# Optimization experiments

Measured on AMD Instinct MI355X. Metric: run time of the kernel, lower is better.

Reference implementation:

```python
import jax, jax.numpy as jnp
import numpy as np

B0, K, H, W = 8, 1, 512, 512
S, CS, NMS, M = 25, 51, 5, 2048
REG_W, COV_POW = 1.0, 0.5

def _gauss_kernel(n):
    x = jnp.linspace(-1.0, 1.0, n)
    g = jnp.exp(-x * x / 0.5)
    return g / g.sum()

def _conv1d2d(x, k1d, horizontal, pad_h, pad_w):
    # x: [B,1,H,W]; replicates torch F.conv2d with the given (possibly asymmetric) padding
    kern = k1d.reshape(1, 1, 1, -1) if horizontal else k1d.reshape(1, 1, -1, 1)
    return jax.lax.conv_general_dilated(x, kern, (1, 1), [(pad_h, pad_h), (pad_w, pad_w)],
                                        dimension_numbers=("NCHW", "OIHW", "NCHW"))

def bilinear_sample(img, pts):
    # img [B,C,H,W], pts [B,N,2] (x,y in [-1,1]); grid_sample bilinear, align_corners=False, zero padding
    Bb, C, Hh, Ww = img.shape
    x = (pts[..., 0] + 1.0) * 0.5 * Ww - 0.5
    y = (pts[..., 1] + 1.0) * 0.5 * Hh - 0.5
    x0 = jnp.floor(x); y0 = jnp.floor(y)
    wx = x - x0; wy = y - y0
    x0i = x0.astype(jnp.int32); y0i = y0.astype(jnp.int32)
    flat = img.reshape(Bb, C, Hh * Ww)
    def tap(yi, xi, w):
        ok = ((yi >= 0) & (yi < Hh) & (xi >= 0) & (xi < Ww)).astype(img.dtype)
        idx = jnp.clip(yi, 0, Hh - 1) * Ww + jnp.clip(xi, 0, Ww - 1)  # [B,N]
        v = jnp.take_along_axis(flat, idx[:, None, :], axis=2)        # [B,C,N]
        return v * (w * ok)[:, None, :]
    return (tap(y0i, x0i, (1 - wy) * (1 - wx)) + tap(y0i, x0i + 1, (1 - wy) * wx)
            + tap(y0i + 1, x0i, wy * (1 - wx)) + tap(y0i + 1, x0i + 1, wy * wx))

def compute_matchability(keypoint_p, has_depth, Bt):
    G = _gauss_kernel(S)
    # NOTE: faithful to original asymmetric padding bug: pad H while convolving along W, then pad W while convolving along H
    s = _conv1d2d(keypoint_p.reshape(Bt, 1, H, W), G, True, S // 2, 0)
    s = _conv1d2d(s, G, False, 0, S // 2)
    log_p_hat = jax.nn.log_softmax(jnp.log(s.reshape(Bt, H * W) + 1e-8), axis=-1)
    sd = _conv1d2d(has_depth.reshape(Bt, 1, H, W), G, True, 0, S // 2)
    sd = _conv1d2d(sd, G, False, S // 2, 0).reshape(Bt, H * W)
    p = sd / sd.sum(-1, keepdims=True)
    return jnp.sum(jnp.where(p > 0, p * (jnp.log(jnp.maximum(p, 1e-30)) - log_p_hat), 0.0), axis=-1)

def sample_keypoints(sm):
    # sm [B,H,W]; coverage-reweighted NMS + top-k (topk=True, subpixel=False)
    wcov = jnp.exp(-jnp.square(jnp.linspace(-2.0, 2.0, CS)))
    ld = _conv1d2d(((sm + 1e-6) * 1e4)[:, None], wcov, True, 0, CS // 2)
    ld = _conv1d2d(ld, wcov, False, CS // 2, 0)[:, 0]
    sm = sm * (ld + 1e-8) ** (-COV_POW)
    p = NMS // 2
    mx = jax.lax.reduce_window(sm, -jnp.inf, jax.lax.max, (1, NMS, NMS), (1, 1, 1),
                               [(0, 0), (p, p), (p, p)])
    sm = sm * (sm == mx)
    _, inds = jax.lax.top_k(sm.reshape(-1, H * W), M)
    xs = (jnp.arange(W) + 0.5) * 2.0 / W - 1.0
    ys = (jnp.arange(H) + 0.5) * 2.0 / H - 1.0
    grid = jnp.stack(jnp.meshgrid(xs, ys, indexing="xy"), axis=-1).reshape(H * W, 2)
    return jnp.take(grid, inds, axis=0)  # [B,M,2] normalized (x,y)

def masked_log_softmax(logits, mask):
    return jax.nn.log_softmax(jnp.where(mask, logits, -1e9), axis=-1)

def _reward(d):
    return jnp.exp(-100.0 * d)

def _forward(scoremap, gt_warp_A2B, gt_warp_B2A, valid_A2B, valid_B2A, has_depth):
    sg = jax.lax.stop_gradient
    lA = scoremap[:B0].reshape(B0, K, H * W)
    lB = scoremap[B0:].reshape(B0, K, H * W)
    logits = jnp.concatenate([lA, lB], 0)                                   # [2B,K,HW]
    kp_p = jax.nn.softmax(logits.reshape(2 * B0, K * H * W), -1).reshape(2 * B0, K, H * W).sum(1)
    match_loss = compute_matchability(kp_p, sg(has_depth), 2 * B0).mean()
    # sparse branch is under torch.set_grad_enabled(False)
    kpts_A = sample_keypoints(sg(kp_p[:B0]).reshape(B0, H, W))
    kpts_B = sample_keypoints(sg(kp_p[B0:]).reshape(B0, H, W))
    kpts_A2B = bilinear_sample(sg(gt_warp_A2B[..., 2:]).transpose(0, 3, 1, 2), kpts_A).transpose(0, 2, 1)
    kpts_B2A = bilinear_sample(sg(gt_warp_B2A[..., 2:]).transpose(0, 3, 1, 2), kpts_B).transpose(0, 2, 1)
    legit_A2B = bilinear_sample(sg(valid_A2B)[:, None], kpts_A)[:, 0] > 0   # [B,M]
    legit_B2A = bilinear_sample(sg(valid_B2A)[:, None], kpts_B)[:, 0] > 0
    dA = jnp.sqrt(jnp.sum(jnp.square(kpts_A2B[:, :, None] - kpts_B[:, None]), -1) + 1e-12).min(-1)
    dB = jnp.sqrt(jnp.sum(jnp.square(kpts_B2A[:, :, None] - kpts_A[:, None]), -1) + 1e-12).min(-1)
    rA = _reward(dA); rB = _reward(dB)
    slA = bilinear_sample(lA.reshape(B0, 1, H, W), kpts_A)[:, 0]            # [B,M]
    slB = bilinear_sample(lB.reshape(B0, 1, H, W), kpts_B)[:, 0]
    lpA = masked_log_softmax(slA, legit_A2B)
    lpB = masked_log_softmax(slB, legit_B2A)
    sparse = -jnp.sum(jnp.where(legit_A2B, rA * lpA, 0.0)) - jnp.sum(jnp.where(legit_B2A, rB * lpB, 0.0))
    return sparse + REG_W * match_loss

def setup_inputs() -> dict:
    key = jax.random.key(0)
    ks = jax.random.split(key, 6)
    scoremap = jax.random.normal(ks[0], (2 * B0, K, H, W), jnp.float32)
    gt_warp_A2B = jax.random.uniform(ks[1], (B0, H, W, 4), jnp.float32, -1.0, 1.0)
    gt_warp_B2A = jax.random.uniform(ks[2], (B0, H, W, 4), jnp.float32, -1.0, 1.0)
    valid_A2B = (jax.random.uniform(ks[3], (B0, H, W)) > 0.3).astype(jnp.float32)
    valid_B2A = (jax.random.uniform(ks[4], (B0, H, W)) > 0.3).astype(jnp.float32)
    has_depth = (jax.random.uniform(ks[5], (2 * B0, H, W)) > 0.3).astype(jnp.float32)
    return dict(scoremap=scoremap, gt_warp_A2B=gt_warp_A2B, gt_warp_B2A=gt_warp_B2A,
                valid_A2B=valid_A2B, valid_B2A=valid_B2A, has_depth=has_depth)

def reference(scoremap, gt_warp_A2B, gt_warp_B2A, valid_A2B, valid_B2A, has_depth):
    return _forward(scoremap, gt_warp_A2B, gt_warp_B2A, valid_A2B, valid_B2A, has_depth)
```

## Files before the change

kernel.cpp:

```cpp
#include <hip/hip_runtime.h>

#define HH 512
#define WW 512
#define HW_ 262144
#define NIMG 16
#define MK 2048
#define CAPB 4096
#define SCAP 32768
#define SBUFN 768

static constexpr size_t OFF_B1    = 16777216;
static constexpr size_t OFF_B2    = 33554432;
static constexpr size_t OFF_SMALL = 50331648;
static constexpr size_t OFF_SEL  = 4194304;
static constexpr size_t OFF_BND  = 4325376;
static constexpr size_t OFF_PP   = 4849664;
static constexpr size_t OFF_WXp  = 5111808;
static constexpr size_t OFF_WYp  = 5242880;
static constexpr size_t OFF_LG   = 5373952;
static constexpr size_t OFF_SL   = 5505024;
static constexpr size_t OFF_PMIN = 5636096;
static constexpr size_t OFF_HIST = 33554432;
static constexpr size_t OFF_SURV = 33554432 + 4194304;

#define CSTRIDE 32

__device__ __forceinline__ float wred64(float v) {
  for (int m = 1; m < 64; m <<= 1) v += __shfl_xor(v, m);
  return v;
}

__device__ __forceinline__ void g25_wave0(float* g) {
  int t = threadIdx.x;
  if (t < 64) {
    float raw = 0.0f;
    if (t < 25) {
      float x = -1.0f + (float)t * (2.0f / 24.0f);
      raw = expf(-(x * x) / 0.5f);
    }
    float s = raw;
    for (int m = 1; m < 64; m <<= 1) s += __shfl_xor(s, m);
    if (t < 25) g[t] = raw / s;
  }
}
__device__ __forceinline__ void w51_wave0(float* wc) {
  int t = threadIdx.x;
  if (t < 51) {
    float x = -2.0f + (float)t * (4.0f / 50.0f);
    wc[t] = expf(-x * x);
  }
}

template<int B>
__device__ __forceinline__ float brsum(float v, float* red) {
  int t = threadIdx.x;
  red[t] = v; __syncthreads();
  for (int s = B >> 1; s > 0; s >>= 1) {
    if (t < s) red[t] += red[t + s];
    __syncthreads();
  }
  float r = red[0]; __syncthreads();
  return r;
}
template<int B>
__device__ __forceinline__ float brmax(float v, float* red) {
  int t = threadIdx.x;
  red[t] = v; __syncthreads();
  for (int s = B >> 1; s > 0; s >>= 1) {
    if (t < s) red[t] = fmaxf(red[t], red[t + s]);
    __syncthreads();
  }
  float r = red[0]; __syncthreads();
  return r;
}

__global__ void __launch_bounds__(256)
k_pre(const float* __restrict__ x, const float* __restrict__ hd, float* A,
      float* sume, float* sumS, float* Zb) {
  __shared__ float g[25];
  __shared__ float red[12];
  int tid = threadIdx.x;
  g25_wave0(g);
  size_t base = (size_t)blockIdx.x * 1024;
  size_t e = base + tid * 4;
  float4 xs = *(const float4*)(x + e);
  float4 hs = *(const float4*)(hd + e);
  __syncthreads();
  int rem = (int)(e & (HW_ - 1));
  int y = rem >> 9, x0 = rem & 511;
  float wv = 0.0f;
  {
    int k0 = y - 499; if (k0 < 0) k0 = 0;
    int k1 = y + 12;  if (k1 > 24) k1 = 24;
    for (int k = k0; k <= k1; k++) wv += g[k];
  }
  float cwv[4], cpv[4];
  {
    int lo = x0 - 487; if (lo < 0) lo = 0;
    int hi = x0;       if (hi > 24) hi = 24;
    float c = 0.0f;
    for (int d = lo; d <= hi; d++) c += g[d];
    cwv[0] = c;
    for (int q = 1; q < 4; q++) {
      int i = x0 + q;
      if (i <= 24) c += g[i];
      if (i >= 488) c -= g[i - 488];
      cwv[q] = c;
    }
  }
  {
    int lo = x0 - 499; if (lo < 0) lo = 0;
    int hi = x0 + 12;  if (hi > 24) hi = 24;
    float c = 0.0f;
    for (int d = lo; d <= hi; d++) c += g[d];
    cpv[0] = c;
    for (int q = 1; q < 4; q++) {
      int i = x0 + q;
      if (i + 12 <= 24) c += g[i + 12];
      if (i >= 500) c -= g[i - 500];
      cpv[q] = c;
    }
  }
  float e0 = expf(xs.x), e1 = expf(xs.y), e2 = expf(xs.z), e3 = expf(xs.w);
  *(float4*)(A + e) = make_float4(e0, e1, e2, e3);
  float r0 = (e0 + e1) + (e2 + e3);
  float r1 = (e0 * cwv[0] + e1 * cwv[1] + e2 * cwv[2] + e3 * cwv[3]) * wv;
  float r2 = (hs.x * cpv[0] + hs.y * cpv[1] + hs.z * cpv[2] + hs.w * cpv[3]) * wv;
  r0 = wred64(r0); r1 = wred64(r1); r2 = wred64(r2);
  int wid = tid >> 6;
  if ((tid & 63) == 0) { red[wid] = r0; red[4 + wid] = r1; red[8 + wid] = r2; }
  __syncthreads();
  if (tid == 0) {
    int img = (int)(base >> 18);
    atomicAdd(&sume[img * CSTRIDE], red[0] + red[1] + red[2] + red[3]);
    atomicAdd(&sumS[img * CSTRIDE], red[4] + red[5] + red[6] + red[7]);
    atomicAdd(&Zb[img * CSTRIDE], red[8] + red[9] + red[10] + red[11]);
  }
}

__global__ void __launch_bounds__(256)
k_hconv(const float* __restrict__ A, const float* __restrict__ hd,
        const float* __restrict__ sume, float* b1, float* b2) {
  __shared__ __align__(16) float ta[512];
  __shared__ __align__(16) float th[536];
  __shared__ float g[25];
  int tid = threadIdx.x;
  int blk = blockIdx.x;
  int img = blk >> 9;
  size_t rowoff = (size_t)blk * 512;
  g25_wave0(g);
  ((float2*)ta)[tid] = *(const float2*)(A + rowoff + tid * 2);
  ((float2*)(th + 12))[tid] = *(const float2*)(hd + rowoff + tid * 2);
  if (tid < 12) { th[tid] = 0.0f; th[524 + tid] = 0.0f; }
  __syncthreads();
  float inv = 1.0f / sume[img * CSTRIDE];
  int j = 2 * tid;
  float v1a = 0.0f, v1b = 0.0f;
  if (tid >= 6 && tid <= 249) {
    float w[26];
#pragma unroll
    for (int d = 0; d < 26; d++) w[d] = ta[j - 12 + d];
#pragma unroll
    for (int d = 0; d < 25; d++) {
      v1a = fmaf(g[d], w[d], v1a);
      v1b = fmaf(g[d], w[d + 1], v1b);
    }
  }
  float v2a = 0.0f, v2b = 0.0f;
  {
    float u[26];
#pragma unroll
    for (int d = 0; d < 26; d++) u[d] = th[j + d];
#pragma unroll
    for (int d = 0; d < 25; d++) {
      v2a = fmaf(g[d], u[d], v2a);
      v2b = fmaf(g[d], u[d + 1], v2b);
    }
  }
  ((float2*)b1)[blk * 256 + tid] = make_float2(v1a * inv, v1b * inv);
  ((float2*)b2)[blk * 256 + tid] = make_float2(v2a, v2b);
}

__global__ void __launch_bounds__(256)
k_match(const float* __restrict__ b1, const float* __restrict__ b2,
        const float* __restrict__ sume, const float* sumS, const float* Zb,
        float* macc) {
  __shared__ float g[25];
  __shared__ float t1[88 * 64];
  __shared__ float t2[88 * 64];
  __shared__ float red4[4];
  g25_wave0(g);
  int blk = blockIdx.x;
  int img = blk >> 6;
  int ty = (blk >> 3) & 7;
  int tx = blk & 7;
  int y0 = ty * 64, x0 = tx * 64;
  const float* base1 = b1 + (size_t)img * HW_;
  const float* base2 = b2 + (size_t)img * HW_;
  for (int i = threadIdx.x; i < 88 * 64; i += 256) {
    int r = i >> 6, c = i & 63;
    int y = y0 + r - 12;
    float v1 = 0.0f, v2 = 0.0f;
    if (y >= 0 && y < 512) {
      size_t o = (size_t)y * 512 + x0 + c;
      v1 = base1[o]; v2 = base2[o];
    }
    t1[i] = v1; t2[i] = v2;
  }
  __syncthreads();
  float Z = Zb[img * CSTRIDE];
  float inv = 1.0f / sume[img * CSTRIDE];
  float logS = logf(sumS[img * CSTRIDE] * inv + (float)HW_ * 1e-8f);
  float acc = 0.0f;
  for (int w = threadIdx.x; w < 1024; w += 256) {
    int rg = w >> 6, c = w & 63;
    int r0 = rg * 4;
    float s[4] = {0.f, 0.f, 0.f, 0.f};
    float d[4] = {0.f, 0.f, 0.f, 0.f};
#pragma unroll
    for (int i = 0; i < 28; i++) {
      float v1 = t1[(r0 + i) * 64 + c];
      float v2 = t2[(r0 + i) * 64 + c];
#pragma unroll
      for (int jj = 0; jj < 4; jj++) {
        if (i >= jj && i - jj < 25) {
          s[jj] = fmaf(g[i - jj], v1, s[jj]);
          d[jj] = fmaf(g[i - jj], v2, d[jj]);
        }
      }
    }
#pragma unroll
    for (int jj = 0; jj < 4; jj++) {
      float p = d[jj] / Z;
      if (p > 0.0f)
        acc += p * (logf(fmaxf(p, 1e-30f)) - (logf(s[jj] + 1e-8f) - logS));
    }
  }
  acc = wred64(acc);
  if ((threadIdx.x & 63) == 0) red4[threadIdx.x >> 6] = acc;
  __syncthreads();
  if (threadIdx.x == 0)
    atomicAdd(macc, red4[0] + red4[1] + red4[2] + red4[3]);
}

__global__ void __launch_bounds__(256)
k_h51(const float* __restrict__ A, const float* __restrict__ sume, float* out) {
  __shared__ float wc[51];
  __shared__ __align__(16) float ta[564];
  int tid = threadIdx.x;
  int blk = blockIdx.x;
  int img = blk >> 9;
  size_t rowoff = (size_t)blk * 512;
  w51_wave0(wc);
  float s1 = 1e4f / sume[img * CSTRIDE];
  for (int i = tid; i < 562; i += 256) {
    int j = i - 25;
    ta[i] = ((unsigned)j < 512u) ? fmaf(A[rowoff + j], s1, 1e-2f) : 0.0f;
  }
  __syncthreads();
  int j = 2 * tid;
  float w[52];
#pragma unroll
  for (int d = 0; d < 52; d++) w[d] = ta[j + d];
  float va = 0.0f, vb = 0.0f;
#pragma unroll
  for (int d = 0; d < 51; d++) {
    va = fmaf(wc[d], w[d], va);
    vb = fmaf(wc[d], w[d + 1], vb);
  }
  ((float2*)out)[blk * 256 + tid] = make_float2(va, vb);
}

__global__ void __launch_bounds__(512)
k_smwnms(const float* __restrict__ A, const float* __restrict__ sume,
         const float* __restrict__ b1,
         unsigned long long* surv, unsigned* scnt, unsigned* hist) {
  __shared__ float wc[51];
  __shared__ float tb1[118 * 68];
  __shared__ float tsm[68 * 68];
  __shared__ unsigned long long sbuf[SBUFN];
  __shared__ unsigned lcnt;
  __shared__ unsigned gbase;
  float* hm = tb1;
  int tid = threadIdx.x;
  w51_wave0(wc);
  if (tid == 0) lcnt = 0;
  int blk = blockIdx.x;
  int img = blk >> 6;
  int ty = (blk >> 3) & 7;
  int tx = blk & 7;
  int y0 = ty * 64, x0 = tx * 64;
  const float* base = b1 + (size_t)img * HW_;
  for (int i = tid; i < 118 * 68; i += 512) {
    int r = i / 68, c = i - r * 68;
    int y = y0 + r - 27, x = x0 + c - 2;
    tb1[i] = (y >= 0 && y < 512 && x >= 0 && x < 512)
                 ? base[(size_t)y * 512 + x] : 0.0f;
  }
  __syncthreads();
  float inv = 1.0f / sume[img * CSTRIDE];
  const float* abase = A + (size_t)img * HW_;
  for (int w = tid; w < 68 * 17; w += 512) {
    int rg = w / 68, c = w - rg * 68;
    int r0 = rg * 4;
    float a[4] = {0.f, 0.f, 0.f, 0.f};
#pragma unroll
    for (int i = 0; i < 54; i++) {
      float v = tb1[(r0 + i) * 68 + c];
#pragma unroll
      for (int jj = 0; jj < 4; jj++) {
        if (i >= jj && i - jj < 51) a[jj] = fmaf(wc[i - jj], v, a[jj]);
      }
    }
#pragma unroll
    for (int jj = 0; jj < 4; jj++) {
      int r = r0 + jj;
      int y = y0 + r - 2, x = x0 + c - 2;
      float res = -3.4e38f;
      if (y >= 0 && y < 512 && x >= 0 && x < 512)
        res = (abase[(size_t)y * 512 + x] * inv) / sqrtf(a[jj] + 1e-8f);
      tsm[r * 68 + c] = res;
    }
  }
  __syncthreads();
  for (int i = tid; i < 68 * 64; i += 512) {
    int r = i >> 6, c = i & 63;
    const float* row = tsm + r * 68 + c;
    float m = fmaxf(fmaxf(row[0], row[1]), fmaxf(row[2], fmaxf(row[3], row[4])));
    hm[i] = m;
  }
  __syncthreads();
  for (int k0 = 0; k0 < 8; k0++) {
    int i = tid + k0 * 512;
    int r = i >> 6, c = i & 63;
    float v = tsm[(r + 2) * 68 + (c + 2)];
    float M = hm[r * 64 + c];
    M = fmaxf(M, hm[(r + 1) * 64 + c]);
    M = fmaxf(M, hm[(r + 2) * 64 + c]);
    M = fmaxf(M, hm[(r + 3) * 64 + c]);
    M = fmaxf(M, hm[(r + 4) * 64 + c]);
    bool keep = (v == M) && (v != 0.0f);
    if (keep) {
      unsigned p = atomicAdd(&lcnt, 1u);
      unsigned bits = __float_as_uint(v);
      unsigned idx = (unsigned)((y0 + r) * 512 + x0 + c);
      if (p < SBUFN)
        sbuf[p] = ((unsigned long long)bits << 32) |
                  (unsigned long long)(idx ^ 0xFFFFFFFFu);
      atomicAdd(&hist[(size_t)img * 65536 + (bits >> 16)], 1u);
    }
  }
  __syncthreads();
  unsigned total = lcnt; if (total > SBUFN) total = SBUFN;
  if (tid == 0) gbase = atomicAdd(&scnt[img * CSTRIDE], total);
  __syncthreads();
  unsigned gb = gbase;
  for (unsigned i = tid; i < total; i += 512) {
    unsigned p = gb + i;
    if (p < SCAP) surv[(size_t)img * SCAP + p] = sbuf[i];
  }
}

__global__ void k_thresh(const unsigned* __restrict__ hist, unsigned* Tb, unsigned* needb) {
  int img = blockIdx.x;
  const unsigned* h = hist + (size_t)img * 65536;
  __shared__ unsigned part[256];
  __shared__ unsigned scan[257];
  int t = threadIdx.x;
  unsigned s = 0;
  for (int k = 0; k < 256; k++) {
    int bin = 65535 - (t * 256 + k);
    s += (bin == 0) ? 0x00100000u : h[bin];
  }
  part[t] = s; __syncthreads();
  if (t == 0) {
    unsigned c = 0;
    for (int k = 0; k < 256; k++) { scan[k] = c; c += part[k]; }
    scan[256] = c;
  }
  __syncthreads();
  unsigned pre = scan[t];
  if (pre < MK && pre + part[t] >= MK) {
    unsigned c = pre;
    for (int k = 0; k < 256; k++) {
      int bin = 65535 - (t * 256 + k);
      unsigned cnt = (bin == 0) ? 0x00100000u : h[bin];
      if (c + cnt >= MK) { Tb[img * CSTRIDE] = (unsigned)bin; needb[img * CSTRIDE] = MK - c; break; }
      c += cnt;
    }
  }
}

__global__ void k_collect(const unsigned long long* __restrict__ surv,
                          const unsigned* __restrict__ scnt,
                          const unsigned* __restrict__ Tb,
                          unsigned* selcnt, unsigned* sel,
                          unsigned* bcnt, unsigned long long* bnd) {
  int blk = blockIdx.x;
  int img = blk >> 7;
  int i = (blk & 127) * 256 + threadIdx.x;
  unsigned cnt = scnt[img * CSTRIDE]; if (cnt > SCAP) cnt = SCAP;
  unsigned long long entry = ((unsigned)i < cnt) ? surv[(size_t)img * SCAP + i] : 0ull;
  unsigned bits = (unsigned)(entry >> 32);
  unsigned bin = bits >> 16;
  unsigned T = Tb[img * CSTRIDE];
  bool ok = (unsigned)i < cnt;
  bool c1 = ok && (bin > T);
  bool c2 = ok && (bin == T);
  int lane = threadIdx.x & 63;
  unsigned long long lowmask = (1ull << lane) - 1ull;

  unsigned long long m1 = __ballot(c1);
  if (m1) {
    int leader = __ffsll(m1) - 1;
    unsigned base = 0;
    if (lane == leader) base = atomicAdd(&selcnt[img * CSTRIDE], (unsigned)__popcll(m1));
    base = __shfl(base, leader);
    if (c1) {
      unsigned p = base + (unsigned)__popcll(m1 & lowmask);
      if (p < MK) sel[img * MK + p] = (unsigned)(entry & 0xFFFFFFFFull) ^ 0xFFFFFFFFu;
    }
  }
  unsigned long long m2 = __ballot(c2);
  if (m2) {
    int leader = __ffsll(m2) - 1;
    unsigned base = 0;
    if (lane == leader) base = atomicAdd(&bcnt[img * CSTRIDE], (unsigned)__popcll(m2));
    base = __shfl(base, leader);
    if (c2) {
      unsigned p = base + (unsigned)__popcll(m2 & lowmask);
      if (p < CAPB) bnd[(size_t)img * CAPB + p] = entry;
    }
  }
}

__global__ void __launch_bounds__(1024)
k_finsel(const unsigned long long* __restrict__ bnd, const unsigned* bcnt,
         const unsigned* needb, const unsigned* selcnt, unsigned* sel) {
  int img = blockIdx.x;
  __shared__ unsigned long long key[CAPB];
  unsigned bn = bcnt[img * CSTRIDE];
  int n = (bn < CAPB) ? (int)bn : CAPB;
  int np2 = 2;
  while (np2 < n) np2 <<= 1;
  int t = threadIdx.x;
  for (int k = t; k < np2; k += 1024)
    key[k] = (k < n) ? bnd[(size_t)img * CAPB + k] : 0ull;
  __syncthreads();
  for (int sz = 2; sz <= np2; sz <<= 1) {
    for (int st = sz >> 1; st > 0; st >>= 1) {
      for (int i = t; i < np2; i += 1024) {
        int l = i ^ st;
        if (l > i) {
          unsigned long long a = key[i], b = key[l];
          bool up = ((i & sz) == 0);
          if (up ? (a < b) : (a > b)) { key[i] = b; key[l] = a; }
        }
      }
      __syncthreads();
    }
  }
  unsigned c1 = selcnt[img * CSTRIDE]; if (c1 > MK) c1 = MK;
  unsigned need = needb[img * CSTRIDE];
  unsigned kk = need; if (kk > MK - c1) kk = MK - c1;
  for (unsigned m = t; m < MK - c1; m += 1024) {
    unsigned v = 0u;
    if (m < kk && m < (unsigned)n)
      v = (unsigned)(key[m] & 0xFFFFFFFFull) ^ 0xFFFFFFFFu;
    sel[img * MK + c1 + m] = v;
  }
}

__global__ void k_prep(const unsigned* __restrict__ sel, const float* __restrict__ scoremap,
                       const float* __restrict__ gtA, const float* __restrict__ gtB,
                       const float* __restrict__ vA, const float* __restrict__ vB,
                       float2* pp, float* wx, float* wy, float* lg, float* sl) {
  int t = blockIdx.x * 256 + threadIdx.x;
  int img = t >> 11;
  unsigned idx = sel[t] & (HW_ - 1);
  int h = idx >> 9, w = idx & 511;
  pp[t] = make_float2((w + 0.5f) * (2.0f / 512.0f) - 1.0f,
                      (h + 0.5f) * (2.0f / 512.0f) - 1.0f);
  int b = (img < 8) ? img : img - 8;
  const float* gt = (img < 8) ? gtA : gtB;
  const float* vv = (img < 8) ? vA : vB;
  size_t pix = (size_t)b * HW_ + idx;
  float2 gxy = *(const float2*)(gt + pix * 4 + 2);
  wx[t] = gxy.x;
  wy[t] = gxy.y;
  lg[t] = (vv[pix] > 0.0f) ? 1.0f : 0.0f;
  sl[t] = scoremap[(size_t)img * HW_ + idx];
}

__global__ void __launch_bounds__(256)
k_mindist(const float2* __restrict__ pp,
          const float* __restrict__ wx, const float* __restrict__ wy,
          float* pmin) {
  __shared__ float2 opp[512];
  int blk = blockIdx.x;
  int img = blk >> 5;
  int qc = (blk >> 2) & 7;
  int oc = blk & 3;
  const float2* ob = pp + (size_t)(img ^ 8) * MK + oc * 512;
  for (int k = threadIdx.x; k < 512; k += 256) opp[k] = ob[k];
  __syncthreads();
  int m = img * MK + qc * 256 + threadIdx.x;
  float ax = wx[m], ay = wy[m];
  float d[8];
#pragma unroll
  for (int u = 0; u < 8; u++) d[u] = 3.4e38f;
  for (int n = 0; n < 512; n += 8) {
#pragma unroll
    for (int u = 0; u < 8; u++) {
      float2 o = opp[n + u];
      float dx = ax - o.x, dy = ay - o.y;
      d[u] = fminf(d[u], fmaf(dx, dx, dy * dy));
    }
  }
  float d2 = fminf(fminf(fminf(d[0], d[1]), fminf(d[2], d[3])),
                   fminf(fminf(d[4], d[5]), fminf(d[6], d[7])));
  pmin[oc * (NIMG * MK) + m] = d2;
}

__global__ void __launch_bounds__(1024)
k_loss(const float* __restrict__ sl, const float* __restrict__ lg,
       const float* __restrict__ pmin, float* sacc) {
  int img = blockIdx.x;
  __shared__ float red[1024];
  int t = threadIdx.x;
  int i0 = img * MK + t, i1 = i0 + 1024;
  float s0 = sl[i0], s1 = sl[i1];
  float g0 = lg[i0], g1 = lg[i1];
  float l0 = (g0 > 0.0f) ? s0 : -1e9f;
  float l1 = (g1 > 0.0f) ? s1 : -1e9f;
  float mx = brmax<1024>(fmaxf(l0, l1), red);
  float se = brsum<1024>(expf(l0 - mx) + expf(l1 - mx), red);
  float lse = mx + logf(se);
  const int ST = NIMG * MK;
  float a = 0.0f;
  if (g0 > 0.0f) {
    float mn = fminf(fminf(pmin[i0], pmin[ST + i0]),
                     fminf(pmin[2 * ST + i0], pmin[3 * ST + i0]));
    float r0 = expf(-100.0f * sqrtf(mn + 1e-12f));
    a += r0 * (s0 - lse);
  }
  if (g1 > 0.0f) {
    float mn = fminf(fminf(pmin[i1], pmin[ST + i1]),
                     fminf(pmin[2 * ST + i1], pmin[3 * ST + i1]));
    float r1 = expf(-100.0f * sqrtf(mn + 1e-12f));
    a += r1 * (s1 - lse);
  }
  float tot = brsum<1024>(a, red);
  if (t == 0) atomicAdd(sacc, -tot);
}

__global__ void k_out(const float* macc, const float* sacc, float* out) {
  out[0] = sacc[0] + macc[0] * (1.0f / 16.0f);
}

extern "C" void kernel_launch(void* const* d_in, const int* in_sizes, int n_in,
                              void* d_out, int out_size, void* d_ws, size_t ws_size,
                              hipStream_t stream) {
  const float* scoremap = (const float*)d_in[0];
  const float* gtA = (const float*)d_in[1];
  const float* gtB = (const float*)d_in[2];
  const float* vA  = (const float*)d_in[3];
  const float* vB  = (const float*)d_in[4];
  const float* hd  = (const float*)d_in[5];

  char* ws = (char*)d_ws;
  float* A  = (float*)(ws);
  float* B1 = (float*)(ws + OFF_B1);

  char* sm = ws + OFF_SMALL;
  float*    sume   = (float*)(sm + 0);
  float*    sumS   = (float*)(sm + 2048);
  float*    Zb     = (float*)(sm + 4096);
  unsigned* Tb     = (unsigned*)(sm + 6144);
  unsigned* needb  = (unsigned*)(sm + 8192);
  unsigned* selcnt = (unsigned*)(sm + 10240);
  unsigned* bcnt   = (unsigned*)(sm + 12288);
  float*    macc   = (float*)(sm + 14336);
  float*    sacc   = (float*)(sm + 14464);
  unsigned* scnt   = (unsigned*)(sm + 16384);

  unsigned* hist = (unsigned*)(ws + OFF_HIST);
  unsigned long long* surv = (unsigned long long*)(ws + OFF_SURV);
  unsigned* sel  = (unsigned*)(ws + OFF_SEL);
  unsigned long long* bnd = (unsigned long long*)(ws + OFF_BND);
  float2* pp = (float2*)(ws + OFF_PP);
  float* wx = (float*)(ws + OFF_WXp);
  float* wy = (float*)(ws + OFF_WYp);
  float* lg = (float*)(ws + OFF_LG);
  float* sl = (float*)(ws + OFF_SL);
  float* pmin = (float*)(ws + OFF_PMIN);
  float* B2 = (float*)(ws + 33554432);

  float* out = (float*)d_out;

  hipMemsetAsync(sm, 0, 32768, stream);

  k_pre<<<4096, 256, 0, stream>>>(scoremap, hd, A, sume, sumS, Zb);

  k_hconv<<<8192, 256, 0, stream>>>(A, hd, sume, B1, B2);
  k_match<<<1024, 256, 0, stream>>>(B1, B2, sume, sumS, Zb, macc);

  k_h51<<<8192, 256, 0, stream>>>(A, sume, B1);
  hipMemsetAsync(ws + OFF_HIST, 0, (size_t)16 * 65536 * 4, stream);

  k_smwnms<<<1024, 512, 0, stream>>>(A, sume, B1, surv, scnt, hist);
  k_thresh<<<16, 256, 0, stream>>>(hist, Tb, needb);
  k_collect<<<2048, 256, 0, stream>>>(surv, scnt, Tb, selcnt, sel, bcnt, bnd);
  k_finsel<<<16, 1024, 0, stream>>>(bnd, bcnt, needb, selcnt, sel);

  k_prep<<<128, 256, 0, stream>>>(sel, scoremap, gtA, gtB, vA, vB, pp, wx, wy, lg, sl);
  k_mindist<<<512, 256, 0, stream>>>(pp, wx, wy, pmin);
  k_loss<<<16, 1024, 0, stream>>>(sl, lg, pmin, sacc);
  k_out<<<1, 1, 0, stream>>>(macc, sacc, out);
}
```

Baseline: 326.3 us.

## Vectorize and register-block the fused vertical blur and NMS kernel

Rewrites k_smwnms so each thread computes a 3x4 register tile of the vertical 51-tap convolution with float4 shared-memory reads and a sliding weight window. The halo load uses float2, and the horizontal and vertical max passes work on four columns per thread. The survivor buffer now aliases the tb1 tile instead of a separate shared array, cutting LDS use, and launch bounds request 6 waves per SIMD. This trades fewer threads active in the conv stage (391 of 512) for fewer LDS loads per FMA, and risks extra register pressure and LDS bank conflicts.

```diff
diff --git a/kernel.cpp b/kernel.cpp
--- a/kernel.cpp
+++ b/kernel.cpp
@@ -271,19 +271,20 @@
   ((float2*)out)[blk * 256 + tid] = make_float2(va, vb);
 }
 
-__global__ void __launch_bounds__(512)
+__global__ void __launch_bounds__(512, 6)
 k_smwnms(const float* __restrict__ A, const float* __restrict__ sume,
          const float* __restrict__ b1,
          unsigned long long* surv, unsigned* scnt, unsigned* hist) {
-  __shared__ float wc[51];
-  __shared__ float tb1[118 * 68];
-  __shared__ float tsm[68 * 68];
-  __shared__ unsigned long long sbuf[SBUFN];
+  __shared__ float wc[53];
+  __shared__ __align__(16) float tb1[119 * 68];
+  __shared__ __align__(16) float tsm[68 * 68];
   __shared__ unsigned lcnt;
   __shared__ unsigned gbase;
   float* hm = tb1;
+  unsigned long long* sbuf = (unsigned long long*)(tb1 + 4352);
   int tid = threadIdx.x;
   w51_wave0(wc);
+  if (tid == 51 || tid == 52) wc[tid] = 0.0f;
   if (tid == 0) lcnt = 0;
   int blk = blockIdx.x;
   int img = blk >> 6;
@@ -291,64 +292,107 @@
   int tx = blk & 7;
   int y0 = ty * 64, x0 = tx * 64;
   const float* base = b1 + (size_t)img * HW_;
-  for (int i = tid; i < 118 * 68; i += 512) {
-    int r = i / 68, c = i - r * 68;
-    int y = y0 + r - 27, x = x0 + c - 2;
-    tb1[i] = (y >= 0 && y < 512 && x >= 0 && x < 512)
-                 ? base[(size_t)y * 512 + x] : 0.0f;
+  for (int i = tid; i < 119 * 34; i += 512) {
+    int r = i / 34, c2 = i - r * 34;
+    int y = y0 + r - 27;
+    int x = x0 + c2 * 2 - 2;
+    float2 v = make_float2(0.0f, 0.0f);
+    if ((unsigned)y < 512u && (unsigned)x < 512u)
+      v = *(const float2*)(base + (size_t)y * 512 + x);
+    *(float2*)(tb1 + r * 68 + c2 * 2) = v;
   }
   __syncthreads();
   float inv = 1.0f / sume[img * CSTRIDE];
   const float* abase = A + (size_t)img * HW_;
-  for (int w = tid; w < 68 * 17; w += 512) {
-    int rg = w / 68, c = w - rg * 68;
-    int r0 = rg * 4;
-    float a[4] = {0.f, 0.f, 0.f, 0.f};
-#pragma unroll
-    for (int i = 0; i < 54; i++) {
-      float v = tb1[(r0 + i) * 68 + c];
-#pragma unroll
-      for (int jj = 0; jj < 4; jj++) {
-        if (i >= jj && i - jj < 51) a[jj] = fmaf(wc[i - jj], v, a[jj]);
+  if (tid < 23 * 17) {
+    int rg = tid / 17, cg = tid - rg * 17;
+    int r0 = rg * 3, c0 = cg * 4;
+    int nr = (r0 <= 65) ? 3 : 2;
+    float a0x = 0.f, a0y = 0.f, a0z = 0.f, a0w = 0.f;
+    float a1x = 0.f, a1y = 0.f, a1z = 0.f, a1w = 0.f;
+    float a2x = 0.f, a2y = 0.f, a2z = 0.f, a2w = 0.f;
+    float w1 = 0.f, w2 = 0.f;
+    const float* tp = tb1 + r0 * 68 + c0;
+#pragma unroll 4
+    for (int i = 0; i < 53; i++) {
+      float4 v = *(const float4*)(tp + i * 68);
+      float w0 = wc[i];
+      a0x = fmaf(w0, v.x, a0x); a0y = fmaf(w0, v.y, a0y);
+      a0z = fmaf(w0, v.z, a0z); a0w = fmaf(w0, v.w, a0w);
+      a1x = fmaf(w1, v.x, a1x); a1y = fmaf(w1, v.y, a1y);
+      a1z = fmaf(w1, v.z, a1z); a1w = fmaf(w1, v.w, a1w);
+      a2x = fmaf(w2, v.x, a2x); a2y = fmaf(w2, v.y, a2y);
+      a2z = fmaf(w2, v.z, a2z); a2w = fmaf(w2, v.w, a2w);
+      w2 = w1; w1 = w0;
+    }
+    auto storerow = [&](int jj, float ax, float ay, float az, float aw) {
+      int r = r0 + jj;
+      int y = y0 + r - 2;
+      int xb = x0 + c0 - 2;
+      float4 res = make_float4(-3.4e38f, -3.4e38f, -3.4e38f, -3.4e38f);
+      if ((unsigned)y < 512u) {
+        const float* ar = abase + (size_t)y * 512;
+        if ((unsigned)xb < 512u) {
+          float2 p = *(const float2*)(ar + xb);
+          res.x = (p.x * inv) / sqrtf(ax + 1e-8f);
+          res.y = (p.y * inv) / sqrtf(ay + 1e-8f);
+        }
+        if ((unsigned)(xb + 2) < 512u) {
+          float2 p = *(const float2*)(ar + xb + 2);
+          res.z = (p.x * inv) / sqrtf(az + 1e-8f);
+          res.w = (p.y * inv) / sqrtf(aw + 1e-8f);
+        }
       }
-    }
-#pragma unroll
-    for (int jj = 0; jj < 4; jj++) {
-      int r = r0 + jj;
-      int y = y0 + r - 2, x = x0 + c - 2;
-      float res = -3.4e38f;
-      if (y >= 0 && y < 512 && x >= 0 && x < 512)
-        res = (abase[(size_t)y * 512 + x] * inv) / sqrtf(a[jj] + 1e-8f);
-      tsm[r * 68 + c] = res;
-    }
-  }
-  __syncthreads();
-  for (int i = tid; i < 68 * 64; i += 512) {
-    int r = i >> 6, c = i & 63;
-    const float* row = tsm + r * 68 + c;
-    float m = fmaxf(fmaxf(row[0], row[1]), fmaxf(row[2], fmaxf(row[3], row[4])));
-    hm[i] = m;
-  }
-  __syncthreads();
-  for (int k0 = 0; k0 < 8; k0++) {
+      *(float4*)(tsm + r * 68 + c0) = res;
+    };
+    storerow(0, a0x, a0y, a0z, a0w);
+    storerow(1, a1x, a1y, a1z, a1w);
+    if (nr == 3) storerow(2, a2x, a2y, a2z, a2w);
+  }
+  __syncthreads();
+  for (int i = tid; i < 68 * 16; i += 512) {
+    int r = i >> 4, cg = i & 15;
+    const float* row = tsm + r * 68 + cg * 4;
+    float4 v0 = *(const float4*)(row);
+    float4 v1 = *(const float4*)(row + 4);
+    float p01 = fmaxf(v0.x, v0.y), p12 = fmaxf(v0.y, v0.z);
+    float p23 = fmaxf(v0.z, v0.w), p34 = fmaxf(v0.w, v1.x);
+    float p45 = fmaxf(v1.x, v1.y), p56 = fmaxf(v1.y, v1.z);
+    float m0 = fmaxf(fmaxf(p01, p23), v1.x);
+    float m1 = fmaxf(fmaxf(p12, p34), v1.y);
+    float m2 = fmaxf(fmaxf(p23, p45), v1.z);
+    float m3 = fmaxf(fmaxf(p34, p56), v1.w);
+    *(float4*)(hm + r * 64 + cg * 4) = make_float4(m0, m1, m2, m3);
+  }
+  __syncthreads();
+  for (int k0 = 0; k0 < 2; k0++) {
     int i = tid + k0 * 512;
-    int r = i >> 6, c = i & 63;
-    float v = tsm[(r + 2) * 68 + (c + 2)];
-    float M = hm[r * 64 + c];
-    M = fmaxf(M, hm[(r + 1) * 64 + c]);
-    M = fmaxf(M, hm[(r + 2) * 64 + c]);
-    M = fmaxf(M, hm[(r + 3) * 64 + c]);
-    M = fmaxf(M, hm[(r + 4) * 64 + c]);
-    bool keep = (v == M) && (v != 0.0f);
-    if (keep) {
-      unsigned p = atomicAdd(&lcnt, 1u);
-      unsigned bits = __float_as_uint(v);
-      unsigned idx = (unsigned)((y0 + r) * 512 + x0 + c);
-      if (p < SBUFN)
-        sbuf[p] = ((unsigned long long)bits << 32) |
-                  (unsigned long long)(idx ^ 0xFFFFFFFFu);
-      atomicAdd(&hist[(size_t)img * 65536 + (bits >> 16)], 1u);
-    }
+    int r = i >> 4, cb = (i & 15) * 4;
+    const float* tp2 = tsm + (r + 2) * 68 + cb + 2;
+    float2 va = *(const float2*)(tp2);
+    float2 vb = *(const float2*)(tp2 + 2);
+    float4 m0 = *(const float4*)(hm + r * 64 + cb);
+    float4 m1 = *(const float4*)(hm + (r + 1) * 64 + cb);
+    float4 m2 = *(const float4*)(hm + (r + 2) * 64 + cb);
+    float4 m3 = *(const float4*)(hm + (r + 3) * 64 + cb);
+    float4 m4 = *(const float4*)(hm + (r + 4) * 64 + cb);
+    float Mx = fmaxf(fmaxf(m0.x, m1.x), fmaxf(fmaxf(m2.x, m3.x), m4.x));
+    float My = fmaxf(fmaxf(m0.y, m1.y), fmaxf(fmaxf(m2.y, m3.y), m4.y));
+    float Mz = fmaxf(fmaxf(m0.z, m1.z), fmaxf(fmaxf(m2.z, m3.z), m4.z));
+    float Mw = fmaxf(fmaxf(m0.w, m1.w), fmaxf(fmaxf(m2.w, m3.w), m4.w));
+    auto keepf = [&](float vk, float Mk, int k) {
+      if (vk == Mk && vk != 0.0f) {
+        unsigned p = atomicAdd(&lcnt, 1u);
+        unsigned bits = __float_as_uint(vk);
+        unsigned idx = (unsigned)((y0 + r) * 512 + x0 + cb + k);
+        if (p < SBUFN)
+          sbuf[p] = ((unsigned long long)bits << 32) |
+                    (unsigned long long)(idx ^ 0xFFFFFFFFu);
+        atomicAdd(&hist[(size_t)img * 65536 + (bits >> 16)], 1u);
+      }
+    };
+    keepf(va.x, Mx, 0); keepf(va.y, My, 1);
+    keepf(vb.x, Mz, 2); keepf(vb.y, Mw, 3);
   }
   __syncthreads();
   unsigned total = lcnt; if (total > SBUFN) total = SBUFN;
```

Result: faster. 318.0 us (-2.5%).
